# Kernel tuning notes

Measured on AMD Instinct MI355X. Metric: run time of the kernel, lower is better.

Reference implementation:

```python
import jax, jax.numpy as jnp
import numpy as np

N, S, R, CM = 1, 128, 256, 256
C, CZ = 32, 128


def setup_inputs() -> dict:
    key = jax.random.key(0)
    k1, k2, k3, k4 = jax.random.split(key, 4)
    return {
        "msa_repr": jax.random.normal(k1, (N, S, R, CM), dtype=jnp.float32),
        "left_proj": jax.random.normal(k2, (CM, C), dtype=jnp.float32) * 0.05,
        "right_proj": jax.random.normal(k3, (CM, C), dtype=jnp.float32) * 0.05,
        "out_proj": jax.random.normal(k4, (C * C, CZ), dtype=jnp.float32) * 0.05,
    }


def reference(msa_repr, left_proj, right_proj, out_proj):
    # msa_repr: [N, S, R, CM]
    # Project to left/right activations and move R before S
    # (equivalent to torch matmul + transpose(-2, -3)).
    a = jnp.einsum("nsrm,mc->nrsc", msa_repr, left_proj)   # [N, R, S, C]
    b = jnp.einsum("nsrm,mc->nrsc", msa_repr, right_proj)  # [N, R, S, C]
    # Outer product contracted over the MSA dim S:
    # outer[n, r, t, c, e] = sum_s a[n, r, s, c] * b[n, t, s, e]
    outer = jnp.einsum("nrsc,ntse->nrtce", a, b)            # [N, R, R, C, C]
    n, r, t = outer.shape[:3]
    outer = outer.reshape(n, r, t, C * C)                   # [N, R, R, C*C]
    # Output projection to pair channels cz
    return outer @ out_proj                                 # [N, R, R, CZ]
```

## Files before the change

### kernel.cpp

```cpp
#include <hip/hip_runtime.h>

typedef __bf16 bf16x8 __attribute__((ext_vector_type(8)));
typedef __bf16 bf16x4 __attribute__((ext_vector_type(4)));
typedef float f32x16 __attribute__((ext_vector_type(16)));
typedef float f32x4 __attribute__((ext_vector_type(4)));

constexpr int S = 128, R = 256, CM = 256, C = 32, CZ = 128;

#define MFMA __builtin_amdgcn_mfma_f32_32x32x16_bf16

__device__ __forceinline__ bf16x4 cvt4(float a, float b, float c, float d) {
    bf16x4 r;
    r[0] = (__bf16)a; r[1] = (__bf16)b; r[2] = (__bf16)c; r[3] = (__bf16)d;
    return r;
}

__global__ __launch_bounds__(256) void k_prep(const float* __restrict__ W,
                                              const float* __restrict__ Lp,
                                              const float* __restrict__ Rp,
                                              __bf16* __restrict__ WTf,
                                              __bf16* __restrict__ WLRT) {
    int b = blockIdx.x;
    if (b < 512) {
        int g = b * 256 + threadIdx.x;
        int cz = g & 127;
        int k = g >> 7;
        int e = k >> 5, c = k & 31;
        float v = W[(size_t)(c * 32 + e) * 128 + cz];
        WTf[((size_t)(k >> 3) * 128 + cz) * 8 + (k & 7)] = (__bf16)v;
    } else {
        int c = b - 512;
        int m = threadIdx.x;
        const float* src = (c < 32) ? Lp : Rp;
        WLRT[(size_t)c * 256 + m] = (__bf16)src[(size_t)m * 32 + (c & 31)];
    }
}

__global__ __launch_bounds__(256) void k_proj(const float* __restrict__ msa,
                                              const __bf16* __restrict__ WLRT,
                                              __bf16* __restrict__ aTf,
                                              __bf16* __restrict__ bTf) {
    __shared__ __align__(16) __bf16 As[32 * 256];
    __shared__ __align__(16) char Pp[2 * 4096];
    const int r = blockIdx.x;
    const int sq = blockIdx.y;
    const int t = threadIdx.x;

#pragma unroll
    for (int it = 0; it < 8; ++it) {
        int idx = it * 256 + t;
        int row = idx >> 6;
        int cg = idx & 63;
        float4 v = *(const float4*)&msa[((size_t)(sq * 32 + row) * R + r) * CM + cg * 4];
        bf16x4 h = cvt4(v.x, v.y, v.z, v.w);
        int P = (cg >> 1) ^ (row & 15);
        *(bf16x4*)((char*)As + row * 512 + P * 16 + (cg & 1) * 8) = h;
    }
    __syncthreads();

    const int w = t >> 6;
    const int l = t & 63;
    const int l31 = t & 31;
    const int kh = (t >> 5) & 1;
    const int sd = w & 1;
    const int ksh = w >> 1;

    f32x16 acc;
#pragma unroll
    for (int q = 0; q < 16; ++q) acc[q] = 0.f;

    const bf16x8* wb = (const bf16x8*)&WLRT[(size_t)(sd * 32 + l31) * 256 + 8 * kh];
    const char* arow = (const char*)As + l31 * 512;

    __builtin_amdgcn_s_setprio(1);
#pragma unroll
    for (int j = 0; j < 8; ++j) {
        int ks = ksh * 8 + j;
        int P = (2 * ks + kh) ^ (l31 & 15);
        bf16x8 af = *(const bf16x8*)(arow + P * 16);
        acc = MFMA(af, wb[2 * ks], acc, 0, 0, 0);
    }
    __builtin_amdgcn_s_setprio(0);

    char* pbase = Pp + (size_t)sd * 4096;
    if (ksh == 1) {
#pragma unroll
        for (int pc = 0; pc < 4; ++pc) {
            f32x4 v;
            v[0] = acc[4 * pc + 0]; v[1] = acc[4 * pc + 1];
            v[2] = acc[4 * pc + 2]; v[3] = acc[4 * pc + 3];
            *(f32x4*)(pbase + ((pc * 64) + l) * 16) = v;
        }
    }
    __syncthreads();
    if (ksh == 0) {
#pragma unroll
        for (int pc = 0; pc < 4; ++pc) {
            f32x4 v = *(const f32x4*)(pbase + ((pc * 64) + l) * 16);
            acc[4 * pc + 0] += v[0]; acc[4 * pc + 1] += v[1];
            acc[4 * pc + 2] += v[2]; acc[4 * pc + 3] += v[3];
        }
        __bf16* dst = sd ? bTf : aTf;
#pragma unroll
        for (int q = 0; q < 4; ++q) {
            size_t base = (size_t)r * 4096 + (size_t)(2 * sq + (q >> 1)) * 512 +
                          (size_t)(q & 1) * 256 + (size_t)l31 * 8 + 4 * kh;
            *(bf16x4*)&dst[base] = cvt4(acc[4 * q + 0], acc[4 * q + 1],
                                        acc[4 * q + 2], acc[4 * q + 3]);
        }
    }
}

__global__ __launch_bounds__(512, 4) void k_main(const __bf16* __restrict__ aTf,
                                                 const __bf16* __restrict__ bTf,
                                                 const __bf16* __restrict__ WTf,
                                                 float* __restrict__ out) {
    __shared__ __align__(16) __bf16 Gs[32 * 1024];

    const int t = threadIdx.x;
    const int w = t >> 6;
    const int l = t & 63;
    const int lane = l & 31;
    const int kh = l >> 5;
    const int r0 = blockIdx.x * 8;
    const int t0 = blockIdx.y * 4;

    const int rg = w >> 1;
    const int tg = w & 1;

    f32x16 acc[2][2];
#pragma unroll
    for (int i = 0; i < 2; ++i)
#pragma unroll
        for (int j = 0; j < 2; ++j)
#pragma unroll
            for (int q = 0; q < 16; ++q) acc[i][j][q] = 0.f;

    const bf16x8* ap0 = (const bf16x8*)aTf + ((size_t)(r0 + 2 * rg + 0) * 512 + kh * 32 + lane);
    const bf16x8* ap1 = (const bf16x8*)aTf + ((size_t)(r0 + 2 * rg + 1) * 512 + kh * 32 + lane);
    const bf16x8* bq0 = (const bf16x8*)bTf + ((size_t)(t0 + 2 * tg + 0) * 512 + kh * 32 + lane);
    const bf16x8* bq1 = (const bf16x8*)bTf + ((size_t)(t0 + 2 * tg + 1) * 512 + kh * 32 + lane);

    bf16x8 Ap[2][2], Bp[2][2];
#define LDA(s, ks) do { \
    Ap[s][0] = ap0[(ks) * 64]; Ap[s][1] = ap1[(ks) * 64]; \
    Bp[s][0] = bq0[(ks) * 64]; Bp[s][1] = bq1[(ks) * 64]; } while (0)
#define PH_A(s) do { \
    __builtin_amdgcn_s_setprio(1); \
    acc[0][0] = MFMA(Ap[s][0], Bp[s][0], acc[0][0], 0, 0, 0); \
    acc[0][1] = MFMA(Ap[s][0], Bp[s][1], acc[0][1], 0, 0, 0); \
    acc[1][0] = MFMA(Ap[s][1], Bp[s][0], acc[1][0], 0, 0, 0); \
    acc[1][1] = MFMA(Ap[s][1], Bp[s][1], acc[1][1], 0, 0, 0); \
    __builtin_amdgcn_s_setprio(0); } while (0)

    LDA(0, 0); LDA(1, 1);
#pragma unroll
    for (int ks = 0; ks < 8; ks += 2) {
        PH_A(0); LDA(0, (ks + 2) & 7);
        PH_A(1); LDA(1, (ks + 3) & 7);
    }

#pragma unroll
    for (int i = 0; i < 2; ++i) {
#pragma unroll
        for (int j = 0; j < 2; ++j) {
            int p = (2 * rg + i) * 4 + 2 * tg + j;
            unsigned prow = (unsigned)p * 2048;
#pragma unroll
            for (int q = 0; q < 4; ++q) {
                int Lc = lane * 4 + q;
                int P = Lc ^ (p & 15) ^ (lane & 7);
                *(bf16x4*)((char*)Gs + prow + (unsigned)P * 16 + kh * 8) =
                    cvt4(acc[i][j][4 * q + 0], acc[i][j][4 * q + 1],
                         acc[i][j][4 * q + 2], acc[i][j][4 * q + 3]);
            }
        }
    }
    __syncthreads();

    const int kq = w >> 1;
    const int ng = w & 1;
    const int czl0 = ng * 64 + lane;
    const int czl1 = czl0 + 32;
    const bf16x8* wb0 = (const bf16x8*)WTf + ((size_t)kh * 128 + czl0);
    const bf16x8* wb1 = (const bf16x8*)WTf + ((size_t)kh * 128 + czl1);
    const unsigned prowG = (unsigned)lane * 2048;
    const int p15 = lane & 15;

    f32x16 o0, o1;
#pragma unroll
    for (int q = 0; q < 16; ++q) { o0[q] = 0.f; o1[q] = 0.f; }

    bf16x8 Wa0, Wa1, Ga, Wb0_, Wb1_, Gb;
#define LDB(W0v, W1v, Gv, kk) do { \
    W0v = wb0[(size_t)(kk) * 256]; \
    W1v = wb1[(size_t)(kk) * 256]; \
    int Lr = (kk) * 2 + kh; \
    int P = Lr ^ p15 ^ ((Lr >> 2) & 7); \
    Gv = *(const bf16x8*)((const char*)Gs + prowG + (unsigned)P * 16); } while (0)
#define PHB(W0v, W1v, Gv) do { \
    __builtin_amdgcn_s_setprio(1); \
    o0 = MFMA(Gv, W0v, o0, 0, 0, 0); \
    o1 = MFMA(Gv, W1v, o1, 0, 0, 0); \
    __builtin_amdgcn_s_setprio(0); } while (0)

    LDB(Wa0, Wa1, Ga, kq * 16);
#pragma unroll
    for (int j = 0; j < 16; j += 2) {
        LDB(Wb0_, Wb1_, Gb, kq * 16 + ((j + 1) & 15));
        PHB(Wa0, Wa1, Ga);
        LDB(Wa0, Wa1, Ga, kq * 16 + ((j + 2) & 15));
        PHB(Wb0_, Wb1_, Gb);
    }
    __syncthreads();

    if (kq > 0) {
        char* pr = (char*)Gs + (size_t)((kq - 1) * 2 + ng) * 8192;
#pragma unroll
        for (int oi = 0; oi < 2; ++oi) {
            const f32x16& ov = oi ? o1 : o0;
#pragma unroll
            for (int pc = 0; pc < 4; ++pc) {
                f32x4 v;
                v[0] = ov[4 * pc + 0]; v[1] = ov[4 * pc + 1];
                v[2] = ov[4 * pc + 2]; v[3] = ov[4 * pc + 3];
                *(f32x4*)(pr + ((oi * 4 + pc) * 64 + l) * 16) = v;
            }
        }
    }
    __syncthreads();

    if (kq == 0) {
#pragma unroll
        for (int kq2 = 1; kq2 < 4; ++kq2) {
            const char* pr = (const char*)Gs + (size_t)((kq2 - 1) * 2 + ng) * 8192;
#pragma unroll
            for (int pc = 0; pc < 4; ++pc) {
                f32x4 v0 = *(const f32x4*)(pr + ((pc) * 64 + l) * 16);
                f32x4 v1 = *(const f32x4*)(pr + ((4 + pc) * 64 + l) * 16);
                o0[4 * pc + 0] += v0[0]; o0[4 * pc + 1] += v0[1];
                o0[4 * pc + 2] += v0[2]; o0[4 * pc + 3] += v0[3];
                o1[4 * pc + 0] += v1[0]; o1[4 * pc + 1] += v1[1];
                o1[4 * pc + 2] += v1[2]; o1[4 * pc + 3] += v1[3];
            }
        }
#pragma unroll
        for (int reg = 0; reg < 16; ++reg) {
            int pl = (reg & 3) + 8 * (reg >> 2) + 4 * kh;
            int pr2 = pl >> 2, pt = pl & 3;
            out[((size_t)(r0 + pr2) * 256 + (t0 + pt)) * 128 + czl0] = o0[reg];
            out[((size_t)(r0 + pr2) * 256 + (t0 + pt)) * 128 + czl1] = o1[reg];
        }
    }
}

extern "C" void kernel_launch(void* const* d_in, const int* in_sizes, int n_in,
                              void* d_out, int out_size, void* d_ws, size_t ws_size,
                              hipStream_t stream) {
    const float* msa = (const float*)d_in[0];
    const float* left = (const float*)d_in[1];
    const float* right = (const float*)d_in[2];
    const float* W = (const float*)d_in[3];

    __bf16* aTf = (__bf16*)d_ws;
    __bf16* bTf = aTf + (size_t)R * 4096;
    __bf16* WTf = bTf + (size_t)R * 4096;
    __bf16* WLRT = WTf + (size_t)128 * 1024;
    float* outp = (float*)d_out;

    k_prep<<<576, 256, 0, stream>>>(W, left, right, WTf, WLRT);
    k_proj<<<dim3(256, 4), 256, 0, stream>>>(msa, WLRT, aTf, bTf);
    k_main<<<dim3(32, 64), 512, 0, stream>>>(aTf, bTf, WTf, outp);
}
```

Before: 62.43 us.

## Double-buffer G tiles and overlap outer-product MFMAs with output projection

Each block now handles two 8x4 pair tiles along t and keeps two LDS G buffers. The outer-product MFMAs for the second tile are interleaved with the output-projection MFMAs of the first. The warp split changes to 4 cz groups by 2 k halves, so the cross-warp reduction shrinks from 4-way to 2-way, and full __syncthreads are replaced by s_barrier with explicit lgkmcnt waits. LDS per block doubles to 128KB and launch bounds drop to 2 blocks per CU, trading occupancy for the intra-block overlap.

```diff
diff --git a/kernel.cpp b/kernel.cpp
--- a/kernel.cpp
+++ b/kernel.cpp
@@ -111,11 +111,12 @@
     }
 }
 
-__global__ __launch_bounds__(512, 4) void k_main(const __bf16* __restrict__ aTf,
+__global__ __launch_bounds__(512, 2) void k_main(const __bf16* __restrict__ aTf,
                                                  const __bf16* __restrict__ bTf,
                                                  const __bf16* __restrict__ WTf,
                                                  float* __restrict__ out) {
-    __shared__ __align__(16) __bf16 Gs[32 * 1024];
+    __shared__ __align__(16) __bf16 Gs0[32768];
+    __shared__ __align__(16) __bf16 Gs1[32768];
 
     const int t = threadIdx.x;
     const int w = t >> 6;
@@ -123,28 +124,34 @@
     const int lane = l & 31;
     const int kh = l >> 5;
     const int r0 = blockIdx.x * 8;
-    const int t0 = blockIdx.y * 4;
-
-    const int rg = w >> 1;
-    const int tg = w & 1;
-
-    f32x16 acc[2][2];
-#pragma unroll
-    for (int i = 0; i < 2; ++i)
-#pragma unroll
-        for (int j = 0; j < 2; ++j)
-#pragma unroll
-            for (int q = 0; q < 16; ++q) acc[i][j][q] = 0.f;
+    const int tb = blockIdx.y * 8;
+
+    const int rg = w & 3;
+    const int tg = w >> 2;
+    const int kq = w >> 2;
+    const int ng = w & 3;
+    const int czl = ng * 32 + lane;
+    const bf16x8* wb = (const bf16x8*)WTf + ((size_t)kh * 128 + czl);
+    const unsigned prowG = (unsigned)lane * 2048;
+    const int p15 = lane & 15;
 
     const bf16x8* ap0 = (const bf16x8*)aTf + ((size_t)(r0 + 2 * rg + 0) * 512 + kh * 32 + lane);
     const bf16x8* ap1 = (const bf16x8*)aTf + ((size_t)(r0 + 2 * rg + 1) * 512 + kh * 32 + lane);
-    const bf16x8* bq0 = (const bf16x8*)bTf + ((size_t)(t0 + 2 * tg + 0) * 512 + kh * 32 + lane);
-    const bf16x8* bq1 = (const bf16x8*)bTf + ((size_t)(t0 + 2 * tg + 1) * 512 + kh * 32 + lane);
-
+    const bf16x8* b00 = (const bf16x8*)bTf + ((size_t)(tb + 2 * tg + 0) * 512 + kh * 32 + lane);
+    const bf16x8* b01 = (const bf16x8*)bTf + ((size_t)(tb + 2 * tg + 1) * 512 + kh * 32 + lane);
+    const bf16x8* b10 = (const bf16x8*)bTf + ((size_t)(tb + 4 + 2 * tg + 0) * 512 + kh * 32 + lane);
+    const bf16x8* b11 = (const bf16x8*)bTf + ((size_t)(tb + 4 + 2 * tg + 1) * 512 + kh * 32 + lane);
+
+    f32x16 acc[2][2];
     bf16x8 Ap[2][2], Bp[2][2];
-#define LDA(s, ks) do { \
+
+#define ZACC() do { \
+    _Pragma("unroll") for (int i = 0; i < 2; ++i) \
+    _Pragma("unroll") for (int j = 0; j < 2; ++j) \
+    _Pragma("unroll") for (int q = 0; q < 16; ++q) acc[i][j][q] = 0.f; } while (0)
+#define LDA_(s, ks, bq0, bq1) do { \
     Ap[s][0] = ap0[(ks) * 64]; Ap[s][1] = ap1[(ks) * 64]; \
-    Bp[s][0] = bq0[(ks) * 64]; Bp[s][1] = bq1[(ks) * 64]; } while (0)
+    Bp[s][0] = (bq0)[(ks) * 64]; Bp[s][1] = (bq1)[(ks) * 64]; } while (0)
 #define PH_A(s) do { \
     __builtin_amdgcn_s_setprio(1); \
     acc[0][0] = MFMA(Ap[s][0], Bp[s][0], acc[0][0], 0, 0, 0); \
@@ -152,104 +159,142 @@
     acc[1][0] = MFMA(Ap[s][1], Bp[s][0], acc[1][0], 0, 0, 0); \
     acc[1][1] = MFMA(Ap[s][1], Bp[s][1], acc[1][1], 0, 0, 0); \
     __builtin_amdgcn_s_setprio(0); } while (0)
-
-    LDA(0, 0); LDA(1, 1);
+#define GWRITE(gb) do { \
+    _Pragma("unroll") for (int i = 0; i < 2; ++i) \
+    _Pragma("unroll") for (int j = 0; j < 2; ++j) { \
+        int p = (2 * rg + i) * 4 + 2 * tg + j; \
+        unsigned prow = (unsigned)p * 2048; \
+        _Pragma("unroll") for (int q = 0; q < 4; ++q) { \
+            int Lc = lane * 4 + q; \
+            int P = Lc ^ (p & 15) ^ (lane & 7); \
+            *(bf16x4*)((char*)(gb) + prow + (unsigned)P * 16 + kh * 8) = \
+                cvt4(acc[i][j][4 * q + 0], acc[i][j][4 * q + 1], \
+                     acc[i][j][4 * q + 2], acc[i][j][4 * q + 3]); \
+        } } } while (0)
+
+    ZACC();
+    LDA_(0, 0, b00, b01); LDA_(1, 1, b00, b01);
 #pragma unroll
     for (int ks = 0; ks < 8; ks += 2) {
-        PH_A(0); LDA(0, (ks + 2) & 7);
-        PH_A(1); LDA(1, (ks + 3) & 7);
-    }
-
-#pragma unroll
-    for (int i = 0; i < 2; ++i) {
-#pragma unroll
-        for (int j = 0; j < 2; ++j) {
-            int p = (2 * rg + i) * 4 + 2 * tg + j;
-            unsigned prow = (unsigned)p * 2048;
-#pragma unroll
-            for (int q = 0; q < 4; ++q) {
-                int Lc = lane * 4 + q;
-                int P = Lc ^ (p & 15) ^ (lane & 7);
-                *(bf16x4*)((char*)Gs + prow + (unsigned)P * 16 + kh * 8) =
-                    cvt4(acc[i][j][4 * q + 0], acc[i][j][4 * q + 1],
-                         acc[i][j][4 * q + 2], acc[i][j][4 * q + 3]);
-            }
-        }
-    }
-    __syncthreads();
-
-    const int kq = w >> 1;
-    const int ng = w & 1;
-    const int czl0 = ng * 64 + lane;
-    const int czl1 = czl0 + 32;
-    const bf16x8* wb0 = (const bf16x8*)WTf + ((size_t)kh * 128 + czl0);
-    const bf16x8* wb1 = (const bf16x8*)WTf + ((size_t)kh * 128 + czl1);
-    const unsigned prowG = (unsigned)lane * 2048;
-    const int p15 = lane & 15;
-
-    f32x16 o0, o1;
-#pragma unroll
-    for (int q = 0; q < 16; ++q) { o0[q] = 0.f; o1[q] = 0.f; }
-
-    bf16x8 Wa0, Wa1, Ga, Wb0_, Wb1_, Gb;
-#define LDB(W0v, W1v, Gv, kk) do { \
-    W0v = wb0[(size_t)(kk) * 256]; \
-    W1v = wb1[(size_t)(kk) * 256]; \
+        PH_A(0); LDA_(0, (ks + 2) & 7, b00, b01);
+        PH_A(1); LDA_(1, (ks + 3) & 7, b00, b01);
+    }
+    GWRITE(Gs0);
+    asm volatile("s_waitcnt lgkmcnt(0)");
+    __builtin_amdgcn_s_barrier();
+
+    bf16x8 Wst[4], Gst[4];
+#define LDB_(s, kk, gb) do { \
+    Wst[s] = wb[(size_t)(kk) * 256]; \
     int Lr = (kk) * 2 + kh; \
     int P = Lr ^ p15 ^ ((Lr >> 2) & 7); \
-    Gv = *(const bf16x8*)((const char*)Gs + prowG + (unsigned)P * 16); } while (0)
-#define PHB(W0v, W1v, Gv) do { \
-    __builtin_amdgcn_s_setprio(1); \
-    o0 = MFMA(Gv, W0v, o0, 0, 0, 0); \
-    o1 = MFMA(Gv, W1v, o1, 0, 0, 0); \
-    __builtin_amdgcn_s_setprio(0); } while (0)
-
-    LDB(Wa0, Wa1, Ga, kq * 16);
-#pragma unroll
-    for (int j = 0; j < 16; j += 2) {
-        LDB(Wb0_, Wb1_, Gb, kq * 16 + ((j + 1) & 15));
-        PHB(Wa0, Wa1, Ga);
-        LDB(Wa0, Wa1, Ga, kq * 16 + ((j + 2) & 15));
-        PHB(Wb0_, Wb1_, Gb);
-    }
-    __syncthreads();
-
-    if (kq > 0) {
-        char* pr = (char*)Gs + (size_t)((kq - 1) * 2 + ng) * 8192;
-#pragma unroll
-        for (int oi = 0; oi < 2; ++oi) {
-            const f32x16& ov = oi ? o1 : o0;
-#pragma unroll
-            for (int pc = 0; pc < 4; ++pc) {
-                f32x4 v;
-                v[0] = ov[4 * pc + 0]; v[1] = ov[4 * pc + 1];
-                v[2] = ov[4 * pc + 2]; v[3] = ov[4 * pc + 3];
-                *(f32x4*)(pr + ((oi * 4 + pc) * 64 + l) * 16) = v;
-            }
-        }
-    }
-    __syncthreads();
-
+    Gst[s] = *(const bf16x8*)((const char*)(gb) + prowG + (unsigned)P * 16); } while (0)
+
+    f32x16 oA, oB;
+#pragma unroll
+    for (int q = 0; q < 16; ++q) { oA[q] = 0.f; oB[q] = 0.f; }
+
+    ZACC();
+    LDA_(0, 0, b10, b11);
+    LDB_(0, kq * 32 + 0, Gs0); LDB_(1, kq * 32 + 1, Gs0);
+    LDB_(2, kq * 32 + 2, Gs0); LDB_(3, kq * 32 + 3, Gs0);
+
+#pragma unroll
+    for (int c = 0; c < 8; ++c) {
+        const int s = c & 1;
+        PH_A(s);
+        if (c < 7) LDA_(s ^ 1, c + 1, b10, b11);
+        __builtin_amdgcn_s_setprio(1);
+        oA = MFMA(Gst[0], Wst[0], oA, 0, 0, 0);
+        __builtin_amdgcn_s_setprio(0);
+        LDB_(0, kq * 32 + ((4 * c + 4) & 31), Gs0);
+        __builtin_amdgcn_s_setprio(1);
+        oB = MFMA(Gst[1], Wst[1], oB, 0, 0, 0);
+        __builtin_amdgcn_s_setprio(0);
+        LDB_(1, kq * 32 + ((4 * c + 5) & 31), Gs0);
+        __builtin_amdgcn_s_setprio(1);
+        oA = MFMA(Gst[2], Wst[2], oA, 0, 0, 0);
+        __builtin_amdgcn_s_setprio(0);
+        LDB_(2, kq * 32 + ((4 * c + 6) & 31), Gs0);
+        __builtin_amdgcn_s_setprio(1);
+        oB = MFMA(Gst[3], Wst[3], oB, 0, 0, 0);
+        __builtin_amdgcn_s_setprio(0);
+        LDB_(3, kq * 32 + ((4 * c + 7) & 31), Gs0);
+    }
+
+    GWRITE(Gs1);
+    asm volatile("s_waitcnt lgkmcnt(0)");
+    __builtin_amdgcn_s_barrier();
+
+    f32x16 osum = oA + oB;
+    if (kq == 1) {
+        char* pb = (char*)Gs0 + (size_t)ng * 4096;
+#pragma unroll
+        for (int pc = 0; pc < 4; ++pc) {
+            f32x4 v;
+            v[0] = osum[4 * pc + 0]; v[1] = osum[4 * pc + 1];
+            v[2] = osum[4 * pc + 2]; v[3] = osum[4 * pc + 3];
+            *(f32x4*)(pb + (pc * 64 + l) * 16) = v;
+        }
+    }
+    asm volatile("s_waitcnt lgkmcnt(0)");
+    __builtin_amdgcn_s_barrier();
     if (kq == 0) {
-#pragma unroll
-        for (int kq2 = 1; kq2 < 4; ++kq2) {
-            const char* pr = (const char*)Gs + (size_t)((kq2 - 1) * 2 + ng) * 8192;
-#pragma unroll
-            for (int pc = 0; pc < 4; ++pc) {
-                f32x4 v0 = *(const f32x4*)(pr + ((pc) * 64 + l) * 16);
-                f32x4 v1 = *(const f32x4*)(pr + ((4 + pc) * 64 + l) * 16);
-                o0[4 * pc + 0] += v0[0]; o0[4 * pc + 1] += v0[1];
-                o0[4 * pc + 2] += v0[2]; o0[4 * pc + 3] += v0[3];
-                o1[4 * pc + 0] += v1[0]; o1[4 * pc + 1] += v1[1];
-                o1[4 * pc + 2] += v1[2]; o1[4 * pc + 3] += v1[3];
-            }
+        const char* pb = (const char*)Gs0 + (size_t)ng * 4096;
+#pragma unroll
+        for (int pc = 0; pc < 4; ++pc) {
+            f32x4 v = *(const f32x4*)(pb + (pc * 64 + l) * 16);
+            osum[4 * pc + 0] += v[0]; osum[4 * pc + 1] += v[1];
+            osum[4 * pc + 2] += v[2]; osum[4 * pc + 3] += v[3];
         }
 #pragma unroll
         for (int reg = 0; reg < 16; ++reg) {
             int pl = (reg & 3) + 8 * (reg >> 2) + 4 * kh;
             int pr2 = pl >> 2, pt = pl & 3;
-            out[((size_t)(r0 + pr2) * 256 + (t0 + pt)) * 128 + czl0] = o0[reg];
-            out[((size_t)(r0 + pr2) * 256 + (t0 + pt)) * 128 + czl1] = o1[reg];
+            out[((size_t)(r0 + pr2) * 256 + (tb + pt)) * 128 + czl] = osum[reg];
+        }
+    }
+
+#pragma unroll
+    for (int q = 0; q < 16; ++q) { oA[q] = 0.f; oB[q] = 0.f; }
+    LDB_(0, kq * 32 + 0, Gs1); LDB_(1, kq * 32 + 1, Gs1);
+    LDB_(2, kq * 32 + 2, Gs1); LDB_(3, kq * 32 + 3, Gs1);
+#pragma unroll
+    for (int j = 0; j < 32; ++j) {
+        const int s = j & 3;
+        __builtin_amdgcn_s_setprio(1);
+        if (j & 1) oB = MFMA(Gst[s], Wst[s], oB, 0, 0, 0);
+        else       oA = MFMA(Gst[s], Wst[s], oA, 0, 0, 0);
+        __builtin_amdgcn_s_setprio(0);
+        LDB_(s, kq * 32 + ((j + 4) & 31), Gs1);
+    }
+
+    osum = oA + oB;
+    if (kq == 1) {
+        char* pb = (char*)Gs0 + 16384 + (size_t)ng * 4096;
+#pragma unroll
+        for (int pc = 0; pc < 4; ++pc) {
+            f32x4 v;
+            v[0] = osum[4 * pc + 0]; v[1] = osum[4 * pc + 1];
+            v[2] = osum[4 * pc + 2]; v[3] = osum[4 * pc + 3];
+            *(f32x4*)(pb + (pc * 64 + l) * 16) = v;
+        }
+    }
+    asm volatile("s_waitcnt lgkmcnt(0)");
+    __builtin_amdgcn_s_barrier();
+    if (kq == 0) {
+        const char* pb = (const char*)Gs0 + 16384 + (size_t)ng * 4096;
+#pragma unroll
+        for (int pc = 0; pc < 4; ++pc) {
+            f32x4 v = *(const f32x4*)(pb + (pc * 64 + l) * 16);
+            osum[4 * pc + 0] += v[0]; osum[4 * pc + 1] += v[1];
+            osum[4 * pc + 2] += v[2]; osum[4 * pc + 3] += v[3];
+        }
+#pragma unroll
+        for (int reg = 0; reg < 16; ++reg) {
+            int pl = (reg & 3) + 8 * (reg >> 2) + 4 * kh;
+            int pr2 = pl >> 2, pt = pl & 3;
+            out[((size_t)(r0 + pr2) * 256 + (tb + 4 + pt)) * 128 + czl] = osum[reg];
         }
     }
 }
@@ -270,5 +315,5 @@
 
     k_prep<<<576, 256, 0, stream>>>(W, left, right, WTf, WLRT);
     k_proj<<<dim3(256, 4), 256, 0, stream>>>(msa, WLRT, aTf, bTf);
-    k_main<<<dim3(32, 64), 512, 0, stream>>>(aTf, bTf, WTf, outp);
-}
+    k_main<<<dim3(32, 32), 512, 0, stream>>>(aTf, bTf, WTf, outp);
+}
```

New measurement: 73.56 us. 17.8% more time.
